# Kernel tuning notes

Measured on AMD Instinct MI355X. Metric: run time of the kernel, lower is better.

## Reference

```python
import jax, jax.numpy as jnp
import numpy as np

N_FEAT = 1024
N_HIDDEN = 31


def _lstm_cell(x, h, c, W_ih, W_hh, b_ih, b_hh):
    # PyTorch LSTMCell: gates ordered i, f, g, o
    gates = x @ W_ih.T + b_ih + h @ W_hh.T + b_hh
    i, f, g, o = jnp.split(gates, 4, axis=-1)
    i = jax.nn.sigmoid(i)
    f = jax.nn.sigmoid(f)
    g = jnp.tanh(g)
    o = jax.nn.sigmoid(o)
    c_new = f * c + i * g
    h_new = o * jnp.tanh(c_new)
    return h_new, c_new


def setup_inputs() -> dict:
    key = jax.random.key(0)
    ks = jax.random.split(key, 12)
    B, T = 64, 512
    s1 = 1.0 / np.sqrt(N_HIDDEN)
    inp = {
        "input": jax.random.normal(ks[0], (B, T, N_FEAT), dtype=jnp.float32),
        "W_ih1": jax.random.uniform(ks[1], (4 * N_HIDDEN, N_FEAT), jnp.float32, -s1, s1),
        "W_hh1": jax.random.uniform(ks[2], (4 * N_HIDDEN, N_HIDDEN), jnp.float32, -s1, s1),
        "b_ih1": jax.random.uniform(ks[3], (4 * N_HIDDEN,), jnp.float32, -s1, s1),
        "b_hh1": jax.random.uniform(ks[4], (4 * N_HIDDEN,), jnp.float32, -s1, s1),
        "W_ih2": jax.random.uniform(ks[5], (4 * N_HIDDEN, N_HIDDEN), jnp.float32, -s1, s1),
        "W_hh2": jax.random.uniform(ks[6], (4 * N_HIDDEN, N_HIDDEN), jnp.float32, -s1, s1),
        "b_ih2": jax.random.uniform(ks[7], (4 * N_HIDDEN,), jnp.float32, -s1, s1),
        "b_hh2": jax.random.uniform(ks[8], (4 * N_HIDDEN,), jnp.float32, -s1, s1),
        "W_lin": jax.random.uniform(ks[9], (N_FEAT, N_HIDDEN), jnp.float32, -s1, s1),
        "b_lin": jax.random.uniform(ks[10], (N_FEAT,), jnp.float32, -s1, s1),
        "future": 16,
    }
    return inp


def reference(input, W_ih1, W_hh1, b_ih1, b_hh1, W_ih2, W_hh2, b_ih2, b_hh2, W_lin, b_lin, future):
    B = input.shape[0]
    h0 = jnp.zeros((B, N_HIDDEN), dtype=input.dtype)
    state0 = (h0, h0, h0, h0)  # h_t, c_t, h_t2, c_t2

    def step(state, x_t):
        h_t, c_t, h_t2, c_t2 = state
        h_t, c_t = _lstm_cell(x_t, h_t, c_t, W_ih1, W_hh1, b_ih1, b_hh1)
        h_t2, c_t2 = _lstm_cell(h_t, h_t2, c_t2, W_ih2, W_hh2, b_ih2, b_hh2)
        out = h_t2 @ W_lin.T + b_lin  # [B, N_FEAT]
        return (h_t, c_t, h_t2, c_t2), out

    # teacher-forced pass over the given sequence
    xs = jnp.swapaxes(input, 0, 1)  # [T, B, F]
    state, outs = jax.lax.scan(step, state0, xs)
    last = outs[-1]

    def fut_step(carry, _):
        state, out = carry
        state, out = step(state, out)
        return (state, out), out

    if future > 0:
        _, fut_outs = jax.lax.scan(fut_step, (state, last), None, length=future)
        outs = jnp.concatenate([outs, fut_outs], axis=0)

    return jnp.swapaxes(outs, 0, 1)  # [B, T+future, N_FEAT]
```

## Files before the change

kernel.cpp:

```cpp
#include <hip/hip_runtime.h>
#include <hip/hip_bf16.h>

#define BB_  64
#define TT_  512
#define FF_  1024
#define HH_  31
#define GG_  124
#define FUT_ 16
#define TTOT_ 528
#define OUT_ROW_ ((size_t)TTOT_ * FF_)

#define PRE1_OFF ((size_t)0)
#define H2A_OFF  (PRE1_OFF + (size_t)TT_*64*128)
#define WT_OFF   (H2A_OFF  + (size_t)TTOT_*64*32)
#define MV_OFF   (WT_OFF   + 31*1024)

__device__ __forceinline__ float rdlane(float v, int k) {
    return __uint_as_float(__builtin_amdgcn_readlane(__float_as_uint(v), k));
}

#define REP31(M) M(0) M(1) M(2) M(3) M(4) M(5) M(6) M(7) M(8) M(9) \
                 M(10) M(11) M(12) M(13) M(14) M(15) M(16) M(17) M(18) M(19) \
                 M(20) M(21) M(22) M(23) M(24) M(25) M(26) M(27) M(28) M(29) M(30)
#define REP16E(M) M(0) M(2) M(4) M(6) M(8) M(10) M(12) M(14) \
                  M(16) M(18) M(20) M(22) M(24) M(26) M(28) M(30)
#define REP15O(M) M(1) M(3) M(5) M(7) M(9) M(11) M(13) M(15) \
                  M(17) M(19) M(21) M(23) M(25) M(27) M(29)

__global__ void k0_prep(const float* __restrict__ Wlin, float* __restrict__ WT) {
    int i = blockIdx.x * 256 + threadIdx.x;
    int j = i / 31;
    int k = i - j * 31;
    WT[k * 1024 + j] = Wlin[i];
}

__global__ __launch_bounds__(64) void k0b_mv(
    const float* __restrict__ Wih1, const float* __restrict__ Wlin,
    const float* __restrict__ blin, float* __restrict__ Mv)
{
    int i = blockIdx.x * 64 + threadIdx.x;
    int g = i >> 5, k = i & 31;
    const float* wr = Wih1 + (size_t)g * FF_;
    float acc = 0.0f;
    if (k < 31) {
#pragma unroll 8
        for (int j = 0; j < FF_; j++) acc += wr[j] * Wlin[j * 31 + k];
    } else {
#pragma unroll 8
        for (int j = 0; j < FF_; j++) acc += wr[j] * blin[j];
    }
    Mv[i] = acc;
}

__global__ __launch_bounds__(256) void k1_pregate(
    const float* __restrict__ X,
    const float* __restrict__ Wih1,
    const float* __restrict__ bih1,
    const float* __restrict__ bhh1,
    float* __restrict__ pre1)
{
    __shared__ __align__(16) float xs[32][64];
    __shared__ __align__(16) float ws[32][128];
    const int tid  = threadIdx.x;
    const int t    = blockIdx.x;
    const int tcol = tid & 31, trow = tid >> 5;
    const int c0 = tcol * 4, r0 = trow * 8;

    float4 acc[8];
#pragma unroll
    for (int r = 0; r < 8; r++) acc[r] = make_float4(0.f, 0.f, 0.f, 0.f);

    for (int kc = 0; kc < 32; ++kc) {
        const int k0 = kc * 32;
#pragma unroll
        for (int p = 0; p < 2; p++) {
            int i = tid + p * 256;
            int r = i >> 3, f = i & 7;
            float4 v = *(const float4*)(X + (size_t)r * TT_ * FF_ + (size_t)t * FF_ + k0 + f * 4);
            xs[f * 4 + 0][r] = v.x; xs[f * 4 + 1][r] = v.y;
            xs[f * 4 + 2][r] = v.z; xs[f * 4 + 3][r] = v.w;
        }
#pragma unroll
        for (int p = 0; p < 4; p++) {
            int i = tid + p * 256;
            int g = i >> 3, f = i & 7;
            float4 v = make_float4(0.f, 0.f, 0.f, 0.f);
            if (g < GG_) v = *(const float4*)(Wih1 + (size_t)g * FF_ + k0 + f * 4);
            ws[f * 4 + 0][g] = v.x; ws[f * 4 + 1][g] = v.y;
            ws[f * 4 + 2][g] = v.z; ws[f * 4 + 3][g] = v.w;
        }
        __syncthreads();
#pragma unroll
        for (int k = 0; k < 32; k++) {
            float4 wv = *(const float4*)&ws[k][c0];
            float4 xa = *(const float4*)&xs[k][r0];
            float4 xb = *(const float4*)&xs[k][r0 + 4];
            float rx[8] = {xa.x, xa.y, xa.z, xa.w, xb.x, xb.y, xb.z, xb.w};
#pragma unroll
            for (int r = 0; r < 8; r++) {
                acc[r].x += rx[r] * wv.x; acc[r].y += rx[r] * wv.y;
                acc[r].z += rx[r] * wv.z; acc[r].w += rx[r] * wv.w;
            }
        }
        __syncthreads();
    }
    float bias[4];
#pragma unroll
    for (int cc = 0; cc < 4; cc++) {
        int c = c0 + cc;
        bias[cc] = (c < GG_) ? (bih1[c] + bhh1[c]) : 0.0f;
    }
#pragma unroll
    for (int r = 0; r < 8; r++) {
        int m = t * 64 + r0 + r;
        float4 o = acc[r];
        o.x += bias[0]; o.y += bias[1]; o.z += bias[2]; o.w += bias[3];
        *(float4*)(pre1 + (size_t)m * 128 + c0) = o;
    }
}

__global__ __attribute__((amdgpu_flat_work_group_size(128, 128), amdgpu_waves_per_eu(1)))
void k2_recur(
    const float* __restrict__ pre1,
    const float* __restrict__ Whh1,
    const float* __restrict__ Wih2,
    const float* __restrict__ Whh2,
    const float* __restrict__ bih1, const float* __restrict__ bhh1,
    const float* __restrict__ bih2, const float* __restrict__ bhh2,
    const float* __restrict__ Mv,
    float* __restrict__ h2a)
{
    __shared__ float gA[2][128];
    __shared__ float g2[2][128];
    const int L  = threadIdx.x;
    const int bb = blockIdx.x;
    const int j  = L & 63;
    const int gc = (L < GG_) ? L : (GG_ - 1);
    const bool isg = (gc >= 62 && gc < 93);
    const bool selhi = (j >= 32);
    const int sidx = selhi ? (j - 32) : j;

#define WLOAD(k) float w1_##k  = Whh1[gc * 31 + k]; \
                 float wi2_##k = Wih2[gc * 31 + k]; \
                 float wh2_##k = Whh2[gc * 31 + k];
    REP31(WLOAD)
#undef WLOAD
#define WPIN(k) asm("" : "+v"(w1_##k), "+v"(wi2_##k), "+v"(wh2_##k));
    REP31(WPIN)
#undef WPIN

    const float b2c = bih2[gc] + bhh2[gc];

    float hv = 0.0f, cv = 0.0f;

    float cur0 = pre1[(size_t)bb * 128 + L];
    float pnxt = pre1[((size_t)1 * 64 + bb) * 128 + L];
    float pnx2 = pre1[((size_t)2 * 64 + bb) * 128 + L];
    {
        float pa0 = cur0, pa1 = 0.0f;
#define DPE(k) { float hk = rdlane(hv, 32 + k); pa0 += w1_##k * hk; }
#define DPO(k) { float hk = rdlane(hv, 32 + k); pa1 += w1_##k * hk; }
        REP16E(DPE)
        REP15O(DPO)
#undef DPE
#undef DPO
        float a = pa0 + pa1;
        float z = isg ? (2.0f * a) : a;
        float s = 1.0f / (1.0f + __expf(-z));
        gA[1][L] = isg ? (2.0f * s - 1.0f) : s;
    }
    __syncthreads();
    {
        const float* gsrc = &gA[1][0];
        float ig = gsrc[sidx];
        float fg = gsrc[sidx + 31];
        float gg = gsrc[sidx + 62];
        float og = gsrc[sidx + 93];
        float cvn = fg * cv + ig * gg;
        float e = __expf(-2.0f * cvn);
        float hvn = og * (2.0f / (1.0f + e) - 1.0f);
        cv = selhi ? cvn : 0.0f;
        hv = selhi ? hvn : 0.0f;
    }

    for (int t = 0; t < TT_ - 1; t++) {
        const int pb = t & 1;
        const float cur = pnxt;
        pnxt = pnx2;
        if (t + 3 < TT_) pnx2 = pre1[((size_t)(t + 3) * 64 + bb) * 128 + L];

        float bi0 = b2c, bi1 = 0.0f, bh0 = 0.0f, bh1 = 0.0f;
        float pa0 = cur, pa1 = 0.0f;
#define DME(k) { float h1k = rdlane(hv, 32 + k); float h2k = rdlane(hv, k); \
                 bi0 += wi2_##k * h1k; bh0 += wh2_##k * h2k; pa0 += w1_##k * h1k; }
#define DMO(k) { float h1k = rdlane(hv, 32 + k); float h2k = rdlane(hv, k); \
                 bi1 += wi2_##k * h1k; bh1 += wh2_##k * h2k; pa1 += w1_##k * h1k; }
        REP16E(DME)
        REP15O(DMO)
#undef DME
#undef DMO
        float b = (bi0 + bi1) + (bh0 + bh1);
        float a = pa0 + pa1;
        {
            float z = isg ? (2.0f * b) : b;
            float s = 1.0f / (1.0f + __expf(-z));
            g2[pb][L] = isg ? (2.0f * s - 1.0f) : s;
        }
        {
            float z = isg ? (2.0f * a) : a;
            float s = 1.0f / (1.0f + __expf(-z));
            gA[pb][L] = isg ? (2.0f * s - 1.0f) : s;
        }
        __syncthreads();
        {
            const float* gsrc = selhi ? &gA[pb][0] : &g2[pb][0];
            float ig = gsrc[sidx];
            float fg = gsrc[sidx + 31];
            float gg = gsrc[sidx + 62];
            float og = gsrc[sidx + 93];
            cv = fg * cv + ig * gg;
            float e = __expf(-2.0f * cv);
            hv = og * (2.0f / (1.0f + e) - 1.0f);
        }
        if (L < HH_) h2a[((size_t)t * 64 + bb) * 32 + L] = hv;
    }

    {
        float bi0 = b2c, bi1 = 0.0f, bh0 = 0.0f, bh1 = 0.0f;
#define DTE(k) { float h1k = rdlane(hv, 32 + k); float h2k = rdlane(hv, k); \
                 bi0 += wi2_##k * h1k; bh0 += wh2_##k * h2k; }
#define DTO(k) { float h1k = rdlane(hv, 32 + k); float h2k = rdlane(hv, k); \
                 bi1 += wi2_##k * h1k; bh1 += wh2_##k * h2k; }
        REP16E(DTE)
        REP15O(DTO)
#undef DTE
#undef DTO
        float b = (bi0 + bi1) + (bh0 + bh1);
        float z = isg ? (2.0f * b) : b;
        float s = 1.0f / (1.0f + __expf(-z));
        g2[1][L] = isg ? (2.0f * s - 1.0f) : s;
    }
    __syncthreads();
    {
        const float* gsrc = &g2[1][0];
        float ig = gsrc[sidx];
        float fg = gsrc[sidx + 31];
        float gg = gsrc[sidx + 62];
        float og = gsrc[sidx + 93];
        float cvn = fg * cv + ig * gg;
        float e = __expf(-2.0f * cvn);
        float hvn = og * (2.0f / (1.0f + e) - 1.0f);
        cv = selhi ? cv : cvn;
        hv = selhi ? hv : hvn;
    }
    if (L < HH_) h2a[((size_t)(TT_ - 1) * 64 + bb) * 32 + L] = hv;

#define MLOAD(k) float m_##k = Mv[gc * 32 + k];
    REP31(MLOAD)
#undef MLOAD
    float m_31 = Mv[gc * 32 + 31];
#define MPIN(k) asm("" : "+v"(m_##k));
    REP31(MPIN)
#undef MPIN
    asm("" : "+v"(m_31));
    const float b1c = bih1[gc] + bhh1[gc];

    for (int sft = 0; sft < FUT_; sft++) {
        float pa0 = b1c + m_31, pa1 = 0.0f;
#define DFE(k) { float h2k = rdlane(hv, k); pa0 += m_##k * h2k; }
#define DFO(k) { float h2k = rdlane(hv, k); pa1 += m_##k * h2k; }
        REP16E(DFE)
        REP15O(DFO)
#undef DFE
#undef DFO
#define DGE(k) { float h1k = rdlane(hv, 32 + k); pa0 += w1_##k * h1k; }
#define DGO(k) { float h1k = rdlane(hv, 32 + k); pa1 += w1_##k * h1k; }
        REP16E(DGE)
        REP15O(DGO)
#undef DGE
#undef DGO
        {
            float a = pa0 + pa1;
            float z = isg ? (2.0f * a) : a;
            float s = 1.0f / (1.0f + __expf(-z));
            gA[0][L] = isg ? (2.0f * s - 1.0f) : s;
        }
        __syncthreads();
        {
            const float* gsrc = &gA[0][0];
            float ig = gsrc[sidx];
            float fg = gsrc[sidx + 31];
            float gg = gsrc[sidx + 62];
            float og = gsrc[sidx + 93];
            float cvn = fg * cv + ig * gg;
            float e = __expf(-2.0f * cvn);
            float hvn = og * (2.0f / (1.0f + e) - 1.0f);
            cv = selhi ? cvn : cv;
            hv = selhi ? hvn : hv;
        }
        float bi0 = b2c, bi1 = 0.0f, bh0 = 0.0f, bh1 = 0.0f;
#define DHE(k) { float h1k = rdlane(hv, 32 + k); float h2k = rdlane(hv, k); \
                 bi0 += wi2_##k * h1k; bh0 += wh2_##k * h2k; }
#define DHO(k) { float h1k = rdlane(hv, 32 + k); float h2k = rdlane(hv, k); \
                 bi1 += wi2_##k * h1k; bh1 += wh2_##k * h2k; }
        REP16E(DHE)
        REP15O(DHO)
#undef DHE
#undef DHO
        {
            float b = (bi0 + bi1) + (bh0 + bh1);
            float z = isg ? (2.0f * b) : b;
            float s = 1.0f / (1.0f + __expf(-z));
            g2[0][L] = isg ? (2.0f * s - 1.0f) : s;
        }
        __syncthreads();
        {
            const float* gsrc = &g2[0][0];
            float ig = gsrc[sidx];
            float fg = gsrc[sidx + 31];
            float gg = gsrc[sidx + 62];
            float og = gsrc[sidx + 93];
            float cvn = fg * cv + ig * gg;
            float e = __expf(-2.0f * cvn);
            float hvn = og * (2.0f / (1.0f + e) - 1.0f);
            cv = selhi ? cv : cvn;
            hv = selhi ? hv : hvn;
        }
        if (L < HH_) h2a[((size_t)(TT_ + sft) * 64 + bb) * 32 + L] = hv;
    }
}

__global__ __launch_bounds__(256) void k3_outlin(
    const float* __restrict__ h2a,
    const float* __restrict__ WT,
    const float* __restrict__ blin,
    float* __restrict__ out)
{
    __shared__ __align__(16) float hl[16][32];
    const int tid = threadIdx.x;
    const int m0  = blockIdx.x * 16;
#pragma unroll
    for (int p = 0; p < 2; p++) {
        int i = tid + p * 256;
        int r = i >> 5, k = i & 31;
        hl[r][k] = h2a[(size_t)(m0 + r) * 32 + k];
    }
    __syncthreads();
    const int c0 = tid * 4;
    float4 bl = *(const float4*)(blin + c0);
    float4 acc[16];
#pragma unroll
    for (int r = 0; r < 16; r++) acc[r] = bl;
    for (int k = 0; k < 31; k++) {
        float4 wv = *(const float4*)(WT + k * 1024 + c0);
#pragma unroll
        for (int r = 0; r < 16; r++) {
            float h = hl[r][k];
            acc[r].x += h * wv.x; acc[r].y += h * wv.y;
            acc[r].z += h * wv.z; acc[r].w += h * wv.w;
        }
    }
    const int t  = m0 >> 6;
    const int b0 = m0 & 63;
#pragma unroll
    for (int r = 0; r < 16; r++) {
        int b = b0 + r;
        *(float4*)(out + (size_t)b * OUT_ROW_ + (size_t)t * FF_ + c0) = acc[r];
    }
}

extern "C" void kernel_launch(void* const* d_in, const int* in_sizes, int n_in,
                              void* d_out, int out_size, void* d_ws, size_t ws_size,
                              hipStream_t stream) {
    (void)in_sizes; (void)n_in; (void)out_size; (void)ws_size;
    const float* X    = (const float*)d_in[0];
    const float* Wih1 = (const float*)d_in[1];
    const float* Whh1 = (const float*)d_in[2];
    const float* bih1 = (const float*)d_in[3];
    const float* bhh1 = (const float*)d_in[4];
    const float* Wih2 = (const float*)d_in[5];
    const float* Whh2 = (const float*)d_in[6];
    const float* bih2 = (const float*)d_in[7];
    const float* bhh2 = (const float*)d_in[8];
    const float* Wlin = (const float*)d_in[9];
    const float* blin = (const float*)d_in[10];

    float* ws   = (float*)d_ws;
    float* pre1 = ws + PRE1_OFF;
    float* h2a  = ws + H2A_OFF;
    float* WT   = ws + WT_OFF;
    float* Mv   = ws + MV_OFF;
    float* out  = (float*)d_out;

    hipLaunchKernelGGL(k0_prep,    dim3(124),  dim3(256), 0, stream, Wlin, WT);
    hipLaunchKernelGGL(k0b_mv,     dim3(62),   dim3(64),  0, stream, Wih1, Wlin, blin, Mv);
    hipLaunchKernelGGL(k1_pregate, dim3(TT_),  dim3(256), 0, stream, X, Wih1, bih1, bhh1, pre1);
    hipLaunchKernelGGL(k2_recur,   dim3(BB_),  dim3(128), 0, stream, pre1, Whh1, Wih2, Whh2,
                       bih1, bhh1, bih2, bhh2, Mv, h2a);
    hipLaunchKernelGGL(k3_outlin,  dim3(TTOT_*4), dim3(256), 0, stream, h2a, WT, blin, out);
}
```

Measured before the change: 809.9 us.

## Pack four batch rows per workgroup in the LSTM recurrence kernel

The recurrent kernel now runs 16 workgroups of 512 threads, each handling four independent batch rows with per-row shared gate buffers, instead of 64 workgroups of 128 threads. The intent is to put more waves on each CU so that latency in the serial readlane/FMA/exp chain can be overlapped across batch rows. The cost is that work is concentrated on fewer CUs, so several waves share each SIMD's issue slots. Every block-wide barrier now waits on all eight waves. The new launch bounds may also cap VGPRs below the roughly 125 pinned weight registers per thread, which risks spills.

```diff
diff --git a/kernel.cpp b/kernel.cpp
--- a/kernel.cpp
+++ b/kernel.cpp
@@ -119,8 +119,7 @@
     }
 }
 
-__global__ __attribute__((amdgpu_flat_work_group_size(128, 128), amdgpu_waves_per_eu(1)))
-void k2_recur(
+__global__ __launch_bounds__(512, 2) void k2_recur(
     const float* __restrict__ pre1,
     const float* __restrict__ Whh1,
     const float* __restrict__ Wih2,
@@ -130,12 +129,14 @@
     const float* __restrict__ Mv,
     float* __restrict__ h2a)
 {
-    __shared__ float gA[2][128];
-    __shared__ float g2[2][128];
-    const int L  = threadIdx.x;
-    const int bb = blockIdx.x;
-    const int j  = L & 63;
-    const int gc = (L < GG_) ? L : (GG_ - 1);
+    __shared__ float gA[4][2][128];
+    __shared__ float g2[4][2][128];
+    const int Lall = threadIdx.x;
+    const int bsl  = Lall >> 7;
+    const int L    = Lall & 127;
+    const int bb   = blockIdx.x * 4 + bsl;
+    const int j    = L & 63;
+    const int gc   = (L < GG_) ? L : (GG_ - 1);
     const bool isg = (gc >= 62 && gc < 93);
     const bool selhi = (j >= 32);
     const int sidx = selhi ? (j - 32) : j;
@@ -167,11 +168,11 @@
         float a = pa0 + pa1;
         float z = isg ? (2.0f * a) : a;
         float s = 1.0f / (1.0f + __expf(-z));
-        gA[1][L] = isg ? (2.0f * s - 1.0f) : s;
+        gA[bsl][1][L] = isg ? (2.0f * s - 1.0f) : s;
     }
     __syncthreads();
     {
-        const float* gsrc = &gA[1][0];
+        const float* gsrc = &gA[bsl][1][0];
         float ig = gsrc[sidx];
         float fg = gsrc[sidx + 31];
         float gg = gsrc[sidx + 62];
@@ -204,16 +205,16 @@
         {
             float z = isg ? (2.0f * b) : b;
             float s = 1.0f / (1.0f + __expf(-z));
-            g2[pb][L] = isg ? (2.0f * s - 1.0f) : s;
+            g2[bsl][pb][L] = isg ? (2.0f * s - 1.0f) : s;
         }
         {
             float z = isg ? (2.0f * a) : a;
             float s = 1.0f / (1.0f + __expf(-z));
-            gA[pb][L] = isg ? (2.0f * s - 1.0f) : s;
+            gA[bsl][pb][L] = isg ? (2.0f * s - 1.0f) : s;
         }
         __syncthreads();
         {
-            const float* gsrc = selhi ? &gA[pb][0] : &g2[pb][0];
+            const float* gsrc = selhi ? &gA[bsl][pb][0] : &g2[bsl][pb][0];
             float ig = gsrc[sidx];
             float fg = gsrc[sidx + 31];
             float gg = gsrc[sidx + 62];
@@ -238,11 +239,11 @@
         float b = (bi0 + bi1) + (bh0 + bh1);
         float z = isg ? (2.0f * b) : b;
         float s = 1.0f / (1.0f + __expf(-z));
-        g2[1][L] = isg ? (2.0f * s - 1.0f) : s;
+        g2[bsl][1][L] = isg ? (2.0f * s - 1.0f) : s;
     }
     __syncthreads();
     {
-        const float* gsrc = &g2[1][0];
+        const float* gsrc = &g2[bsl][1][0];
         float ig = gsrc[sidx];
         float fg = gsrc[sidx + 31];
         float gg = gsrc[sidx + 62];
@@ -283,11 +284,11 @@
             float a = pa0 + pa1;
             float z = isg ? (2.0f * a) : a;
             float s = 1.0f / (1.0f + __expf(-z));
-            gA[0][L] = isg ? (2.0f * s - 1.0f) : s;
+            gA[bsl][0][L] = isg ? (2.0f * s - 1.0f) : s;
         }
         __syncthreads();
         {
-            const float* gsrc = &gA[0][0];
+            const float* gsrc = &gA[bsl][0][0];
             float ig = gsrc[sidx];
             float fg = gsrc[sidx + 31];
             float gg = gsrc[sidx + 62];
@@ -311,11 +312,11 @@
             float b = (bi0 + bi1) + (bh0 + bh1);
             float z = isg ? (2.0f * b) : b;
             float s = 1.0f / (1.0f + __expf(-z));
-            g2[0][L] = isg ? (2.0f * s - 1.0f) : s;
+            g2[bsl][0][L] = isg ? (2.0f * s - 1.0f) : s;
         }
         __syncthreads();
         {
-            const float* gsrc = &g2[0][0];
+            const float* gsrc = &g2[bsl][0][0];
             float ig = gsrc[sidx];
             float fg = gsrc[sidx + 31];
             float gg = gsrc[sidx + 62];
@@ -395,7 +396,7 @@
     hipLaunchKernelGGL(k0_prep,    dim3(124),  dim3(256), 0, stream, Wlin, WT);
     hipLaunchKernelGGL(k0b_mv,     dim3(62),   dim3(64),  0, stream, Wih1, Wlin, blin, Mv);
     hipLaunchKernelGGL(k1_pregate, dim3(TT_),  dim3(256), 0, stream, X, Wih1, bih1, bhh1, pre1);
-    hipLaunchKernelGGL(k2_recur,   dim3(BB_),  dim3(128), 0, stream, pre1, Whh1, Wih2, Whh2,
+    hipLaunchKernelGGL(k2_recur,   dim3(BB_/4), dim3(512), 0, stream, pre1, Whh1, Wih2, Whh2,
                        bih1, bhh1, bih2, bhh2, Mv, h2a);
     hipLaunchKernelGGL(k3_outlin,  dim3(TTOT_*4), dim3(256), 0, stream, h2a, WT, blin, out);
 }
```

Measured after the change: 939.7 us. 1.16x slower.

## Fuse prep kernels into pregate launch and enlarge GEMM and output-linear tiles

Applied to the files above, without the earlier changes.

Merges the Wlin transpose, the Mv precompute and the input pregate GEMM into one heterogeneous launch, using block ranges to dispatch the different roles. The pregate GEMM now handles two timesteps per block with 8 output columns per thread, so each loaded Wih1 tile is reused across twice as many rows. The output linear kernel processes 32 rows per block instead of 16. The aim is fewer launches and more weight reuse, at the cost of higher register pressure (64 and 128 accumulator floats) and fewer blocks for parallelism.

```diff
diff --git a/kernel.cpp b/kernel.cpp
--- a/kernel.cpp
+++ b/kernel.cpp
@@ -27,95 +27,107 @@
 #define REP15O(M) M(1) M(3) M(5) M(7) M(9) M(11) M(13) M(15) \
                   M(17) M(19) M(21) M(23) M(25) M(27) M(29)
 
-__global__ void k0_prep(const float* __restrict__ Wlin, float* __restrict__ WT) {
-    int i = blockIdx.x * 256 + threadIdx.x;
-    int j = i / 31;
-    int k = i - j * 31;
-    WT[k * 1024 + j] = Wlin[i];
-}
-
-__global__ __launch_bounds__(64) void k0b_mv(
-    const float* __restrict__ Wih1, const float* __restrict__ Wlin,
-    const float* __restrict__ blin, float* __restrict__ Mv)
-{
-    int i = blockIdx.x * 64 + threadIdx.x;
-    int g = i >> 5, k = i & 31;
-    const float* wr = Wih1 + (size_t)g * FF_;
-    float acc = 0.0f;
-    if (k < 31) {
-#pragma unroll 8
-        for (int j = 0; j < FF_; j++) acc += wr[j] * Wlin[j * 31 + k];
-    } else {
-#pragma unroll 8
-        for (int j = 0; j < FF_; j++) acc += wr[j] * blin[j];
-    }
-    Mv[i] = acc;
-}
-
-__global__ __launch_bounds__(256) void k1_pregate(
+__global__ __launch_bounds__(256) void k_front(
     const float* __restrict__ X,
     const float* __restrict__ Wih1,
     const float* __restrict__ bih1,
     const float* __restrict__ bhh1,
-    float* __restrict__ pre1)
+    const float* __restrict__ Wlin,
+    const float* __restrict__ blin,
+    float* __restrict__ pre1,
+    float* __restrict__ WT,
+    float* __restrict__ Mv)
 {
-    __shared__ __align__(16) float xs[32][64];
+    __shared__ __align__(16) float xs[32][128];
     __shared__ __align__(16) float ws[32][128];
-    const int tid  = threadIdx.x;
-    const int t    = blockIdx.x;
-    const int tcol = tid & 31, trow = tid >> 5;
-    const int c0 = tcol * 4, r0 = trow * 8;
-
-    float4 acc[8];
-#pragma unroll
-    for (int r = 0; r < 8; r++) acc[r] = make_float4(0.f, 0.f, 0.f, 0.f);
-
-    for (int kc = 0; kc < 32; ++kc) {
-        const int k0 = kc * 32;
-#pragma unroll
-        for (int p = 0; p < 2; p++) {
-            int i = tid + p * 256;
-            int r = i >> 3, f = i & 7;
-            float4 v = *(const float4*)(X + (size_t)r * TT_ * FF_ + (size_t)t * FF_ + k0 + f * 4);
-            xs[f * 4 + 0][r] = v.x; xs[f * 4 + 1][r] = v.y;
-            xs[f * 4 + 2][r] = v.z; xs[f * 4 + 3][r] = v.w;
-        }
-#pragma unroll
-        for (int p = 0; p < 4; p++) {
-            int i = tid + p * 256;
-            int g = i >> 3, f = i & 7;
-            float4 v = make_float4(0.f, 0.f, 0.f, 0.f);
-            if (g < GG_) v = *(const float4*)(Wih1 + (size_t)g * FF_ + k0 + f * 4);
-            ws[f * 4 + 0][g] = v.x; ws[f * 4 + 1][g] = v.y;
-            ws[f * 4 + 2][g] = v.z; ws[f * 4 + 3][g] = v.w;
-        }
-        __syncthreads();
-#pragma unroll
-        for (int k = 0; k < 32; k++) {
-            float4 wv = *(const float4*)&ws[k][c0];
-            float4 xa = *(const float4*)&xs[k][r0];
-            float4 xb = *(const float4*)&xs[k][r0 + 4];
-            float rx[8] = {xa.x, xa.y, xa.z, xa.w, xb.x, xb.y, xb.z, xb.w};
-#pragma unroll
-            for (int r = 0; r < 8; r++) {
-                acc[r].x += rx[r] * wv.x; acc[r].y += rx[r] * wv.y;
-                acc[r].z += rx[r] * wv.z; acc[r].w += rx[r] * wv.w;
+    const int blk = blockIdx.x;
+    const int tid = threadIdx.x;
+
+    if (blk < 256) {
+        const int t0   = blk * 2;
+        const int tcol = tid & 15, trow = tid >> 4;
+        const int c0 = tcol * 8, r0 = trow * 8;
+
+        float4 a0[8], a1[8];
+#pragma unroll
+        for (int r = 0; r < 8; r++) { a0[r] = make_float4(0.f,0.f,0.f,0.f); a1[r] = a0[r]; }
+
+        for (int kc = 0; kc < 32; ++kc) {
+            const int k0f = kc * 32;
+#pragma unroll
+            for (int p = 0; p < 4; p++) {
+                int i = tid + p * 256;
+                int r = i >> 3, f = i & 7;
+                int bb = r & 63, tt = t0 + (r >> 6);
+                float4 v = *(const float4*)(X + (size_t)bb * TT_ * FF_ + (size_t)tt * FF_ + k0f + f * 4);
+                xs[f * 4 + 0][r] = v.x; xs[f * 4 + 1][r] = v.y;
+                xs[f * 4 + 2][r] = v.z; xs[f * 4 + 3][r] = v.w;
             }
-        }
-        __syncthreads();
-    }
-    float bias[4];
-#pragma unroll
-    for (int cc = 0; cc < 4; cc++) {
-        int c = c0 + cc;
-        bias[cc] = (c < GG_) ? (bih1[c] + bhh1[c]) : 0.0f;
-    }
-#pragma unroll
-    for (int r = 0; r < 8; r++) {
-        int m = t * 64 + r0 + r;
-        float4 o = acc[r];
-        o.x += bias[0]; o.y += bias[1]; o.z += bias[2]; o.w += bias[3];
-        *(float4*)(pre1 + (size_t)m * 128 + c0) = o;
+#pragma unroll
+            for (int p = 0; p < 4; p++) {
+                int i = tid + p * 256;
+                int g = i >> 3, f = i & 7;
+                float4 v = make_float4(0.f, 0.f, 0.f, 0.f);
+                if (g < GG_) v = *(const float4*)(Wih1 + (size_t)g * FF_ + k0f + f * 4);
+                ws[f * 4 + 0][g] = v.x; ws[f * 4 + 1][g] = v.y;
+                ws[f * 4 + 2][g] = v.z; ws[f * 4 + 3][g] = v.w;
+            }
+            __syncthreads();
+#pragma unroll
+            for (int k = 0; k < 32; k++) {
+                float4 wv0 = *(const float4*)&ws[k][c0];
+                float4 wv1 = *(const float4*)&ws[k][c0 + 4];
+                float4 xa  = *(const float4*)&xs[k][r0];
+                float4 xb  = *(const float4*)&xs[k][r0 + 4];
+                float rx[8] = {xa.x, xa.y, xa.z, xa.w, xb.x, xb.y, xb.z, xb.w};
+#pragma unroll
+                for (int r = 0; r < 8; r++) {
+                    a0[r].x += rx[r] * wv0.x; a0[r].y += rx[r] * wv0.y;
+                    a0[r].z += rx[r] * wv0.z; a0[r].w += rx[r] * wv0.w;
+                    a1[r].x += rx[r] * wv1.x; a1[r].y += rx[r] * wv1.y;
+                    a1[r].z += rx[r] * wv1.z; a1[r].w += rx[r] * wv1.w;
+                }
+            }
+            __syncthreads();
+        }
+        float bias0[4], bias1[4];
+#pragma unroll
+        for (int cc = 0; cc < 4; cc++) {
+            int c = c0 + cc;
+            bias0[cc] = (c < GG_) ? (bih1[c] + bhh1[c]) : 0.0f;
+            c = c0 + 4 + cc;
+            bias1[cc] = (c < GG_) ? (bih1[c] + bhh1[c]) : 0.0f;
+        }
+#pragma unroll
+        for (int r = 0; r < 8; r++) {
+            int row = r0 + r;
+            int m = (t0 + (row >> 6)) * 64 + (row & 63);
+            float4 o0 = a0[r], o1 = a1[r];
+            o0.x += bias0[0]; o0.y += bias0[1]; o0.z += bias0[2]; o0.w += bias0[3];
+            o1.x += bias1[0]; o1.y += bias1[1]; o1.z += bias1[2]; o1.w += bias1[3];
+            *(float4*)(pre1 + (size_t)m * 128 + c0)     = o0;
+            *(float4*)(pre1 + (size_t)m * 128 + c0 + 4) = o1;
+        }
+    } else if (blk < 380) {
+        int i = (blk - 256) * 256 + tid;
+        int j = i / 31;
+        int k = i - j * 31;
+        WT[k * 1024 + j] = Wlin[i];
+    } else {
+        int idx = (blk - 380) * 256 + tid;
+        if (idx < GG_ * 32) {
+            int g = idx >> 5, k = idx & 31;
+            const float* wr = Wih1 + (size_t)g * FF_;
+            float acc = 0.0f;
+            if (k < 31) {
+#pragma unroll 8
+                for (int j = 0; j < FF_; j++) acc += wr[j] * Wlin[j * 31 + k];
+            } else {
+#pragma unroll 8
+                for (int j = 0; j < FF_; j++) acc += wr[j] * blin[j];
+            }
+            Mv[idx] = acc;
+        }
     }
 }
 
@@ -336,11 +348,11 @@
     const float* __restrict__ blin,
     float* __restrict__ out)
 {
-    __shared__ __align__(16) float hl[16][32];
+    __shared__ __align__(16) float hl[32][32];
     const int tid = threadIdx.x;
-    const int m0  = blockIdx.x * 16;
-#pragma unroll
-    for (int p = 0; p < 2; p++) {
+    const int m0  = blockIdx.x * 32;
+#pragma unroll
+    for (int p = 0; p < 4; p++) {
         int i = tid + p * 256;
         int r = i >> 5, k = i & 31;
         hl[r][k] = h2a[(size_t)(m0 + r) * 32 + k];
@@ -348,13 +360,13 @@
     __syncthreads();
     const int c0 = tid * 4;
     float4 bl = *(const float4*)(blin + c0);
-    float4 acc[16];
-#pragma unroll
-    for (int r = 0; r < 16; r++) acc[r] = bl;
+    float4 acc[32];
+#pragma unroll
+    for (int r = 0; r < 32; r++) acc[r] = bl;
     for (int k = 0; k < 31; k++) {
         float4 wv = *(const float4*)(WT + k * 1024 + c0);
 #pragma unroll
-        for (int r = 0; r < 16; r++) {
+        for (int r = 0; r < 32; r++) {
             float h = hl[r][k];
             acc[r].x += h * wv.x; acc[r].y += h * wv.y;
             acc[r].z += h * wv.z; acc[r].w += h * wv.w;
@@ -363,7 +375,7 @@
     const int t  = m0 >> 6;
     const int b0 = m0 & 63;
 #pragma unroll
-    for (int r = 0; r < 16; r++) {
+    for (int r = 0; r < 32; r++) {
         int b = b0 + r;
         *(float4*)(out + (size_t)b * OUT_ROW_ + (size_t)t * FF_ + c0) = acc[r];
     }
@@ -392,10 +404,9 @@
     float* Mv   = ws + MV_OFF;
     float* out  = (float*)d_out;
 
-    hipLaunchKernelGGL(k0_prep,    dim3(124),  dim3(256), 0, stream, Wlin, WT);
-    hipLaunchKernelGGL(k0b_mv,     dim3(62),   dim3(64),  0, stream, Wih1, Wlin, blin, Mv);
-    hipLaunchKernelGGL(k1_pregate, dim3(TT_),  dim3(256), 0, stream, X, Wih1, bih1, bhh1, pre1);
-    hipLaunchKernelGGL(k2_recur,   dim3(BB_),  dim3(128), 0, stream, pre1, Whh1, Wih2, Whh2,
+    hipLaunchKernelGGL(k_front,   dim3(396),    dim3(256), 0, stream,
+                       X, Wih1, bih1, bhh1, Wlin, blin, pre1, WT, Mv);
+    hipLaunchKernelGGL(k2_recur,  dim3(BB_),    dim3(128), 0, stream, pre1, Whh1, Wih2, Whh2,
                        bih1, bhh1, bih2, bhh2, Mv, h2a);
-    hipLaunchKernelGGL(k3_outlin,  dim3(TTOT_*4), dim3(256), 0, stream, h2a, WT, blin, out);
+    hipLaunchKernelGGL(k3_outlin, dim3(TTOT_*2), dim3(256), 0, stream, h2a, WT, blin, out);
 }
```

Result: faster. 776.8 us (-4.1%).

## Fuse pregate GEMM and recurrence into one kernel with flag-based overlap

Applied to the files above, without the earlier changes.

Merges the weight-prep, Mv precompute, input pregate GEMM and LSTM recurrence into one launch. Blocks 0-511 produce pregates per timestep and signal per-group atomic counters with release semantics. Blocks 512-575 run the recurrence and spin on those counters, so the sequential recurrence can start while later pregates are still being computed. This removes the serialization between the GEMM and the recurrence and cuts launch count. The output-projection kernel is also retiled to 32 rows per block. The risks are spin-wait overhead, consumer-before-producer scheduling hazards, and register pressure from the 256-thread launch bound on the recurrence path.

```diff
diff --git a/kernel.cpp b/kernel.cpp
--- a/kernel.cpp
+++ b/kernel.cpp
@@ -14,9 +14,20 @@
 #define H2A_OFF  (PRE1_OFF + (size_t)TT_*64*128)
 #define WT_OFF   (H2A_OFF  + (size_t)TTOT_*64*32)
 #define MV_OFF   (WT_OFF   + 31*1024)
+#define FLG_OFF  (MV_OFF   + 124*32)
+
+#define NPROD 512
+#define KBLK  64
+#define NBLK  (NPROD + KBLK)
 
 __device__ __forceinline__ float rdlane(float v, int k) {
     return __uint_as_float(__builtin_amdgcn_readlane(__float_as_uint(v), k));
+}
+__device__ __forceinline__ int aload_acq(int* p) {
+    return __hip_atomic_load(p, __ATOMIC_ACQUIRE, __HIP_MEMORY_SCOPE_AGENT);
+}
+__device__ __forceinline__ void aadd_rel(int* p, int v) {
+    __hip_atomic_fetch_add(p, v, __ATOMIC_RELEASE, __HIP_MEMORY_SCOPE_AGENT);
 }
 
 #define REP31(M) M(0) M(1) M(2) M(3) M(4) M(5) M(6) M(7) M(8) M(9) \
@@ -27,267 +38,174 @@
 #define REP15O(M) M(1) M(3) M(5) M(7) M(9) M(11) M(13) M(15) \
                   M(17) M(19) M(21) M(23) M(25) M(27) M(29)
 
-__global__ void k0_prep(const float* __restrict__ Wlin, float* __restrict__ WT) {
-    int i = blockIdx.x * 256 + threadIdx.x;
-    int j = i / 31;
-    int k = i - j * 31;
-    WT[k * 1024 + j] = Wlin[i];
-}
-
-__global__ __launch_bounds__(64) void k0b_mv(
-    const float* __restrict__ Wih1, const float* __restrict__ Wlin,
-    const float* __restrict__ blin, float* __restrict__ Mv)
-{
-    int i = blockIdx.x * 64 + threadIdx.x;
-    int g = i >> 5, k = i & 31;
-    const float* wr = Wih1 + (size_t)g * FF_;
-    float acc = 0.0f;
-    if (k < 31) {
-#pragma unroll 8
-        for (int j = 0; j < FF_; j++) acc += wr[j] * Wlin[j * 31 + k];
-    } else {
-#pragma unroll 8
-        for (int j = 0; j < FF_; j++) acc += wr[j] * blin[j];
-    }
-    Mv[i] = acc;
-}
-
-__global__ __launch_bounds__(256) void k1_pregate(
+__global__ void k_zero(int* flg) {
+    if (threadIdx.x < 128) flg[threadIdx.x] = 0;
+}
+
+__global__ __launch_bounds__(256) void k_fused(
     const float* __restrict__ X,
     const float* __restrict__ Wih1,
-    const float* __restrict__ bih1,
-    const float* __restrict__ bhh1,
-    float* __restrict__ pre1)
-{
-    __shared__ __align__(16) float xs[32][64];
-    __shared__ __align__(16) float ws[32][128];
-    const int tid  = threadIdx.x;
-    const int t    = blockIdx.x;
-    const int tcol = tid & 31, trow = tid >> 5;
-    const int c0 = tcol * 4, r0 = trow * 8;
-
-    float4 acc[8];
-#pragma unroll
-    for (int r = 0; r < 8; r++) acc[r] = make_float4(0.f, 0.f, 0.f, 0.f);
-
-    for (int kc = 0; kc < 32; ++kc) {
-        const int k0 = kc * 32;
-#pragma unroll
-        for (int p = 0; p < 2; p++) {
-            int i = tid + p * 256;
-            int r = i >> 3, f = i & 7;
-            float4 v = *(const float4*)(X + (size_t)r * TT_ * FF_ + (size_t)t * FF_ + k0 + f * 4);
-            xs[f * 4 + 0][r] = v.x; xs[f * 4 + 1][r] = v.y;
-            xs[f * 4 + 2][r] = v.z; xs[f * 4 + 3][r] = v.w;
-        }
-#pragma unroll
-        for (int p = 0; p < 4; p++) {
-            int i = tid + p * 256;
-            int g = i >> 3, f = i & 7;
-            float4 v = make_float4(0.f, 0.f, 0.f, 0.f);
-            if (g < GG_) v = *(const float4*)(Wih1 + (size_t)g * FF_ + k0 + f * 4);
-            ws[f * 4 + 0][g] = v.x; ws[f * 4 + 1][g] = v.y;
-            ws[f * 4 + 2][g] = v.z; ws[f * 4 + 3][g] = v.w;
-        }
-        __syncthreads();
-#pragma unroll
-        for (int k = 0; k < 32; k++) {
-            float4 wv = *(const float4*)&ws[k][c0];
-            float4 xa = *(const float4*)&xs[k][r0];
-            float4 xb = *(const float4*)&xs[k][r0 + 4];
-            float rx[8] = {xa.x, xa.y, xa.z, xa.w, xb.x, xb.y, xb.z, xb.w};
-#pragma unroll
-            for (int r = 0; r < 8; r++) {
-                acc[r].x += rx[r] * wv.x; acc[r].y += rx[r] * wv.y;
-                acc[r].z += rx[r] * wv.z; acc[r].w += rx[r] * wv.w;
-            }
-        }
-        __syncthreads();
-    }
-    float bias[4];
-#pragma unroll
-    for (int cc = 0; cc < 4; cc++) {
-        int c = c0 + cc;
-        bias[cc] = (c < GG_) ? (bih1[c] + bhh1[c]) : 0.0f;
-    }
-#pragma unroll
-    for (int r = 0; r < 8; r++) {
-        int m = t * 64 + r0 + r;
-        float4 o = acc[r];
-        o.x += bias[0]; o.y += bias[1]; o.z += bias[2]; o.w += bias[3];
-        *(float4*)(pre1 + (size_t)m * 128 + c0) = o;
-    }
-}
-
-__global__ __attribute__((amdgpu_flat_work_group_size(128, 128), amdgpu_waves_per_eu(1)))
-void k2_recur(
-    const float* __restrict__ pre1,
     const float* __restrict__ Whh1,
     const float* __restrict__ Wih2,
     const float* __restrict__ Whh2,
     const float* __restrict__ bih1, const float* __restrict__ bhh1,
     const float* __restrict__ bih2, const float* __restrict__ bhh2,
-    const float* __restrict__ Mv,
-    float* __restrict__ h2a)
+    const float* __restrict__ Wlin,
+    const float* __restrict__ blin,
+    float* __restrict__ pre1,
+    float* __restrict__ h2a,
+    float* __restrict__ WT,
+    float* __restrict__ Mv,
+    int*   __restrict__ flg)
 {
-    __shared__ float gA[2][128];
-    __shared__ float g2[2][128];
-    const int L  = threadIdx.x;
-    const int bb = blockIdx.x;
-    const int j  = L & 63;
-    const int gc = (L < GG_) ? L : (GG_ - 1);
-    const bool isg = (gc >= 62 && gc < 93);
-    const bool selhi = (j >= 32);
-    const int sidx = selhi ? (j - 32) : j;
+    __shared__ __align__(16) float smem[6144];
+    int* pre_grp = flg;
+    int* mv_cnt  = flg + 64;
+    const int blk = blockIdx.x;
+    const int tid = threadIdx.x;
+
+    if (blk < NPROD) {
+        const int t = blk;
+        {
+            float (*xs)[64]  = (float(*)[64])smem;
+            float (*ws)[128] = (float(*)[128])(smem + 2048);
+            const int tcol = tid & 31, trow = tid >> 5;
+            const int c0 = tcol * 4, r0 = trow * 8;
+
+            float4 acc[8];
+#pragma unroll
+            for (int r = 0; r < 8; r++) acc[r] = make_float4(0.f, 0.f, 0.f, 0.f);
+
+            for (int kc = 0; kc < 32; ++kc) {
+                const int k0 = kc * 32;
+#pragma unroll
+                for (int p = 0; p < 2; p++) {
+                    int i = tid + p * 256;
+                    int r = i >> 3, f = i & 7;
+                    float4 v = *(const float4*)(X + (size_t)r * TT_ * FF_ + (size_t)t * FF_ + k0 + f * 4);
+                    xs[f * 4 + 0][r] = v.x; xs[f * 4 + 1][r] = v.y;
+                    xs[f * 4 + 2][r] = v.z; xs[f * 4 + 3][r] = v.w;
+                }
+#pragma unroll
+                for (int p = 0; p < 4; p++) {
+                    int i = tid + p * 256;
+                    int g = i >> 3, f = i & 7;
+                    float4 v = make_float4(0.f, 0.f, 0.f, 0.f);
+                    if (g < GG_) v = *(const float4*)(Wih1 + (size_t)g * FF_ + k0 + f * 4);
+                    ws[f * 4 + 0][g] = v.x; ws[f * 4 + 1][g] = v.y;
+                    ws[f * 4 + 2][g] = v.z; ws[f * 4 + 3][g] = v.w;
+                }
+                __syncthreads();
+#pragma unroll
+                for (int k = 0; k < 32; k++) {
+                    float4 wv = *(const float4*)&ws[k][c0];
+                    float4 xa = *(const float4*)&xs[k][r0];
+                    float4 xb = *(const float4*)&xs[k][r0 + 4];
+                    float rx[8] = {xa.x, xa.y, xa.z, xa.w, xb.x, xb.y, xb.z, xb.w};
+#pragma unroll
+                    for (int r = 0; r < 8; r++) {
+                        acc[r].x += rx[r] * wv.x; acc[r].y += rx[r] * wv.y;
+                        acc[r].z += rx[r] * wv.z; acc[r].w += rx[r] * wv.w;
+                    }
+                }
+                __syncthreads();
+            }
+            float bias[4];
+#pragma unroll
+            for (int cc = 0; cc < 4; cc++) {
+                int c = c0 + cc;
+                bias[cc] = (c < GG_) ? (bih1[c] + bhh1[c]) : 0.0f;
+            }
+#pragma unroll
+            for (int r = 0; r < 8; r++) {
+                int m = t * 64 + r0 + r;
+                float4 o = acc[r];
+                o.x += bias[0]; o.y += bias[1]; o.z += bias[2]; o.w += bias[3];
+                *(float4*)(pre1 + (size_t)m * 128 + c0) = o;
+            }
+        }
+        __syncthreads();
+        if (tid == 0) aadd_rel(&pre_grp[t >> 3], 1);
+
+        if (t < 124) {
+            int i = t * 256 + tid;
+            int j = i / 31;
+            int k = i - j * 31;
+            WT[k * 1024 + j] = Wlin[i];
+        } else if (t < 140) {
+            int idx = (t - 124) * 256 + tid;
+            if (idx < GG_ * 32) {
+                int g = idx >> 5, k = idx & 31;
+                const float* wr = Wih1 + (size_t)g * FF_;
+                float acc = 0.0f;
+                if (k < 31) {
+#pragma unroll 8
+                    for (int j = 0; j < FF_; j++) acc += wr[j] * Wlin[j * 31 + k];
+                } else {
+#pragma unroll 8
+                    for (int j = 0; j < FF_; j++) acc += wr[j] * blin[j];
+                }
+                Mv[idx] = acc;
+            }
+            __syncthreads();
+            if (tid == 0) aadd_rel(mv_cnt, 1);
+        }
+        return;
+    }
+
+    if (tid >= 128) {
+        __syncthreads();
+        for (int t = 0; t < TT_ - 1; t++) __syncthreads();
+        __syncthreads();
+        for (int s = 0; s < FUT_; s++) { __syncthreads(); __syncthreads(); }
+        return;
+    }
+
+    {
+        const int L  = tid;
+        const int bb = blk - NPROD;
+        const int j  = L & 63;
+        const int gc = (L < GG_) ? L : (GG_ - 1);
+        const bool isg = (gc >= 62 && gc < 93);
+        const bool selhi = (j >= 32);
+        const int sidx = selhi ? (j - 32) : j;
+        float (*gA)[128] = (float(*)[128])smem;
+        float (*g2)[128] = (float(*)[128])(smem + 256);
 
 #define WLOAD(k) float w1_##k  = Whh1[gc * 31 + k]; \
                  float wi2_##k = Wih2[gc * 31 + k]; \
                  float wh2_##k = Whh2[gc * 31 + k];
-    REP31(WLOAD)
+        REP31(WLOAD)
 #undef WLOAD
 #define WPIN(k) asm("" : "+v"(w1_##k), "+v"(wi2_##k), "+v"(wh2_##k));
-    REP31(WPIN)
+        REP31(WPIN)
 #undef WPIN
 
-    const float b2c = bih2[gc] + bhh2[gc];
-
-    float hv = 0.0f, cv = 0.0f;
-
-    float cur0 = pre1[(size_t)bb * 128 + L];
-    float pnxt = pre1[((size_t)1 * 64 + bb) * 128 + L];
-    float pnx2 = pre1[((size_t)2 * 64 + bb) * 128 + L];
-    {
-        float pa0 = cur0, pa1 = 0.0f;
+        const float b2c = bih2[gc] + bhh2[gc];
+        float hv = 0.0f, cv = 0.0f;
+        int rg = 0;
+
+        while (aload_acq(&pre_grp[0]) < 8) __builtin_amdgcn_s_sleep(8);
+        rg = 1;
+        float cur0 = pre1[(size_t)bb * 128 + L];
+        float pnxt = pre1[((size_t)1 * 64 + bb) * 128 + L];
+        float pnx2 = pre1[((size_t)2 * 64 + bb) * 128 + L];
+        {
+            float pa0 = cur0, pa1 = 0.0f;
 #define DPE(k) { float hk = rdlane(hv, 32 + k); pa0 += w1_##k * hk; }
 #define DPO(k) { float hk = rdlane(hv, 32 + k); pa1 += w1_##k * hk; }
-        REP16E(DPE)
-        REP15O(DPO)
+            REP16E(DPE)
+            REP15O(DPO)
 #undef DPE
 #undef DPO
-        float a = pa0 + pa1;
-        float z = isg ? (2.0f * a) : a;
-        float s = 1.0f / (1.0f + __expf(-z));
-        gA[1][L] = isg ? (2.0f * s - 1.0f) : s;
-    }
-    __syncthreads();
-    {
-        const float* gsrc = &gA[1][0];
-        float ig = gsrc[sidx];
-        float fg = gsrc[sidx + 31];
-        float gg = gsrc[sidx + 62];
-        float og = gsrc[sidx + 93];
-        float cvn = fg * cv + ig * gg;
-        float e = __expf(-2.0f * cvn);
-        float hvn = og * (2.0f / (1.0f + e) - 1.0f);
-        cv = selhi ? cvn : 0.0f;
-        hv = selhi ? hvn : 0.0f;
-    }
-
-    for (int t = 0; t < TT_ - 1; t++) {
-        const int pb = t & 1;
-        const float cur = pnxt;
-        pnxt = pnx2;
-        if (t + 3 < TT_) pnx2 = pre1[((size_t)(t + 3) * 64 + bb) * 128 + L];
-
-        float bi0 = b2c, bi1 = 0.0f, bh0 = 0.0f, bh1 = 0.0f;
-        float pa0 = cur, pa1 = 0.0f;
-#define DME(k) { float h1k = rdlane(hv, 32 + k); float h2k = rdlane(hv, k); \
-                 bi0 += wi2_##k * h1k; bh0 += wh2_##k * h2k; pa0 += w1_##k * h1k; }
-#define DMO(k) { float h1k = rdlane(hv, 32 + k); float h2k = rdlane(hv, k); \
-                 bi1 += wi2_##k * h1k; bh1 += wh2_##k * h2k; pa1 += w1_##k * h1k; }
-        REP16E(DME)
-        REP15O(DMO)
-#undef DME
-#undef DMO
-        float b = (bi0 + bi1) + (bh0 + bh1);
-        float a = pa0 + pa1;
-        {
-            float z = isg ? (2.0f * b) : b;
-            float s = 1.0f / (1.0f + __expf(-z));
-            g2[pb][L] = isg ? (2.0f * s - 1.0f) : s;
-        }
-        {
-            float z = isg ? (2.0f * a) : a;
-            float s = 1.0f / (1.0f + __expf(-z));
-            gA[pb][L] = isg ? (2.0f * s - 1.0f) : s;
-        }
-        __syncthreads();
-        {
-            const float* gsrc = selhi ? &gA[pb][0] : &g2[pb][0];
-            float ig = gsrc[sidx];
-            float fg = gsrc[sidx + 31];
-            float gg = gsrc[sidx + 62];
-            float og = gsrc[sidx + 93];
-            cv = fg * cv + ig * gg;
-            float e = __expf(-2.0f * cv);
-            hv = og * (2.0f / (1.0f + e) - 1.0f);
-        }
-        if (L < HH_) h2a[((size_t)t * 64 + bb) * 32 + L] = hv;
-    }
-
-    {
-        float bi0 = b2c, bi1 = 0.0f, bh0 = 0.0f, bh1 = 0.0f;
-#define DTE(k) { float h1k = rdlane(hv, 32 + k); float h2k = rdlane(hv, k); \
-                 bi0 += wi2_##k * h1k; bh0 += wh2_##k * h2k; }
-#define DTO(k) { float h1k = rdlane(hv, 32 + k); float h2k = rdlane(hv, k); \
-                 bi1 += wi2_##k * h1k; bh1 += wh2_##k * h2k; }
-        REP16E(DTE)
-        REP15O(DTO)
-#undef DTE
-#undef DTO
-        float b = (bi0 + bi1) + (bh0 + bh1);
-        float z = isg ? (2.0f * b) : b;
-        float s = 1.0f / (1.0f + __expf(-z));
-        g2[1][L] = isg ? (2.0f * s - 1.0f) : s;
-    }
-    __syncthreads();
-    {
-        const float* gsrc = &g2[1][0];
-        float ig = gsrc[sidx];
-        float fg = gsrc[sidx + 31];
-        float gg = gsrc[sidx + 62];
-        float og = gsrc[sidx + 93];
-        float cvn = fg * cv + ig * gg;
-        float e = __expf(-2.0f * cvn);
-        float hvn = og * (2.0f / (1.0f + e) - 1.0f);
-        cv = selhi ? cv : cvn;
-        hv = selhi ? hv : hvn;
-    }
-    if (L < HH_) h2a[((size_t)(TT_ - 1) * 64 + bb) * 32 + L] = hv;
-
-#define MLOAD(k) float m_##k = Mv[gc * 32 + k];
-    REP31(MLOAD)
-#undef MLOAD
-    float m_31 = Mv[gc * 32 + 31];
-#define MPIN(k) asm("" : "+v"(m_##k));
-    REP31(MPIN)
-#undef MPIN
-    asm("" : "+v"(m_31));
-    const float b1c = bih1[gc] + bhh1[gc];
-
-    for (int sft = 0; sft < FUT_; sft++) {
-        float pa0 = b1c + m_31, pa1 = 0.0f;
-#define DFE(k) { float h2k = rdlane(hv, k); pa0 += m_##k * h2k; }
-#define DFO(k) { float h2k = rdlane(hv, k); pa1 += m_##k * h2k; }
-        REP16E(DFE)
-        REP15O(DFO)
-#undef DFE
-#undef DFO
-#define DGE(k) { float h1k = rdlane(hv, 32 + k); pa0 += w1_##k * h1k; }
-#define DGO(k) { float h1k = rdlane(hv, 32 + k); pa1 += w1_##k * h1k; }
-        REP16E(DGE)
-        REP15O(DGO)
-#undef DGE
-#undef DGO
-        {
             float a = pa0 + pa1;
             float z = isg ? (2.0f * a) : a;
             float s = 1.0f / (1.0f + __expf(-z));
-            gA[0][L] = isg ? (2.0f * s - 1.0f) : s;
+            gA[1][L] = isg ? (2.0f * s - 1.0f) : s;
         }
         __syncthreads();
         {
-            const float* gsrc = &gA[0][0];
+            const float* gsrc = &gA[1][0];
             float ig = gsrc[sidx];
             float fg = gsrc[sidx + 31];
             float gg = gsrc[sidx + 62];
@@ -295,27 +213,77 @@
             float cvn = fg * cv + ig * gg;
             float e = __expf(-2.0f * cvn);
             float hvn = og * (2.0f / (1.0f + e) - 1.0f);
-            cv = selhi ? cvn : cv;
-            hv = selhi ? hvn : hv;
-        }
-        float bi0 = b2c, bi1 = 0.0f, bh0 = 0.0f, bh1 = 0.0f;
-#define DHE(k) { float h1k = rdlane(hv, 32 + k); float h2k = rdlane(hv, k); \
+            cv = selhi ? cvn : 0.0f;
+            hv = selhi ? hvn : 0.0f;
+        }
+
+        for (int t = 0; t < TT_ - 1; t++) {
+            const int pb = t & 1;
+            const float cur = pnxt;
+            pnxt = pnx2;
+            if (t + 3 < TT_) {
+                const int gneed = (t + 3) >> 3;
+                while (rg <= gneed) {
+                    if (aload_acq(&pre_grp[rg]) == 8) rg++;
+                    else __builtin_amdgcn_s_sleep(2);
+                }
+                pnx2 = pre1[((size_t)(t + 3) * 64 + bb) * 128 + L];
+            }
+
+            float bi0 = b2c, bi1 = 0.0f, bh0 = 0.0f, bh1 = 0.0f;
+            float pa0 = cur, pa1 = 0.0f;
+#define DME(k) { float h1k = rdlane(hv, 32 + k); float h2k = rdlane(hv, k); \
+                 bi0 += wi2_##k * h1k; bh0 += wh2_##k * h2k; pa0 += w1_##k * h1k; }
+#define DMO(k) { float h1k = rdlane(hv, 32 + k); float h2k = rdlane(hv, k); \
+                 bi1 += wi2_##k * h1k; bh1 += wh2_##k * h2k; pa1 += w1_##k * h1k; }
+            REP16E(DME)
+            REP15O(DMO)
+#undef DME
+#undef DMO
+            float b = (bi0 + bi1) + (bh0 + bh1);
+            float a = pa0 + pa1;
+            {
+                float z = isg ? (2.0f * b) : b;
+                float s = 1.0f / (1.0f + __expf(-z));
+                g2[pb][L] = isg ? (2.0f * s - 1.0f) : s;
+            }
+            {
+                float z = isg ? (2.0f * a) : a;
+                float s = 1.0f / (1.0f + __expf(-z));
+                gA[pb][L] = isg ? (2.0f * s - 1.0f) : s;
+            }
+            __syncthreads();
+            {
+                const float* gsrc = selhi ? &gA[pb][0] : &g2[pb][0];
+                float ig = gsrc[sidx];
+                float fg = gsrc[sidx + 31];
+                float gg = gsrc[sidx + 62];
+                float og = gsrc[sidx + 93];
+                cv = fg * cv + ig * gg;
+                float e = __expf(-2.0f * cv);
+                hv = og * (2.0f / (1.0f + e) - 1.0f);
+            }
+            if (L < HH_) h2a[((size_t)t * 64 + bb) * 32 + L] = hv;
+        }
+
+        {
+            float bi0 = b2c, bi1 = 0.0f, bh0 = 0.0f, bh1 = 0.0f;
+#define DTE(k) { float h1k = rdlane(hv, 32 + k); float h2k = rdlane(hv, k); \
                  bi0 += wi2_##k * h1k; bh0 += wh2_##k * h2k; }
-#define DHO(k) { float h1k = rdlane(hv, 32 + k); float h2k = rdlane(hv, k); \
+#define DTO(k) { float h1k = rdlane(hv, 32 + k); float h2k = rdlane(hv, k); \
                  bi1 += wi2_##k * h1k; bh1 += wh2_##k * h2k; }
-        REP16E(DHE)
-        REP15O(DHO)
-#undef DHE
-#undef DHO
-        {
+            REP16E(DTE)
+            REP15O(DTO)
+#undef DTE
+#undef DTO
             float b = (bi0 + bi1) + (bh0 + bh1);
             float z = isg ? (2.0f * b) : b;
             float s = 1.0f / (1.0f + __expf(-z));
-            g2[0][L] = isg ? (2.0f * s - 1.0f) : s;
+            g2[1][L] = isg ? (2.0f * s - 1.0f) : s;
         }
         __syncthreads();
         {
-            const float* gsrc = &g2[0][0];
+            const float* gsrc = &g2[1][0];
             float ig = gsrc[sidx];
             float fg = gsrc[sidx + 31];
             float gg = gsrc[sidx + 62];
@@ -326,7 +294,82 @@
             cv = selhi ? cv : cvn;
             hv = selhi ? hv : hvn;
         }
-        if (L < HH_) h2a[((size_t)(TT_ + sft) * 64 + bb) * 32 + L] = hv;
+        if (L < HH_) h2a[((size_t)(TT_ - 1) * 64 + bb) * 32 + L] = hv;
+
+        while (aload_acq(mv_cnt) < 16) __builtin_amdgcn_s_sleep(2);
+#define MLOAD(k) float m_##k = Mv[gc * 32 + k];
+        REP31(MLOAD)
+#undef MLOAD
+        float m_31 = Mv[gc * 32 + 31];
+#define MPIN(k) asm("" : "+v"(m_##k));
+        REP31(MPIN)
+#undef MPIN
+        asm("" : "+v"(m_31));
+        const float b1c = bih1[gc] + bhh1[gc];
+
+        for (int sft = 0; sft < FUT_; sft++) {
+            float pa0 = b1c + m_31, pa1 = 0.0f;
+#define DFE(k) { float h2k = rdlane(hv, k); pa0 += m_##k * h2k; }
+#define DFO(k) { float h2k = rdlane(hv, k); pa1 += m_##k * h2k; }
+            REP16E(DFE)
+            REP15O(DFO)
+#undef DFE
+#undef DFO
+#define DGE(k) { float h1k = rdlane(hv, 32 + k); pa0 += w1_##k * h1k; }
+#define DGO(k) { float h1k = rdlane(hv, 32 + k); pa1 += w1_##k * h1k; }
+            REP16E(DGE)
+            REP15O(DGO)
+#undef DGE
+#undef DGO
+            {
+                float a = pa0 + pa1;
+                float z = isg ? (2.0f * a) : a;
+                float s = 1.0f / (1.0f + __expf(-z));
+                gA[0][L] = isg ? (2.0f * s - 1.0f) : s;
+            }
+            __syncthreads();
+            {
+                const float* gsrc = &gA[0][0];
+                float ig = gsrc[sidx];
+                float fg = gsrc[sidx + 31];
+                float gg = gsrc[sidx + 62];
+                float og = gsrc[sidx + 93];
+                float cvn = fg * cv + ig * gg;
+                float e = __expf(-2.0f * cvn);
+                float hvn = og * (2.0f / (1.0f + e) - 1.0f);
+                cv = selhi ? cvn : cv;
+                hv = selhi ? hvn : hv;
+            }
+            float bi0 = b2c, bi1 = 0.0f, bh0 = 0.0f, bh1 = 0.0f;
+#define DHE(k) { float h1k = rdlane(hv, 32 + k); float h2k = rdlane(hv, k); \
+                 bi0 += wi2_##k * h1k; bh0 += wh2_##k * h2k; }
+#define DHO(k) { float h1k = rdlane(hv, 32 + k); float h2k = rdlane(hv, k); \
+                 bi1 += wi2_##k * h1k; bh1 += wh2_##k * h2k; }
+            REP16E(DHE)
+            REP15O(DHO)
+#undef DHE
+#undef DHO
+            {
+                float b = (bi0 + bi1) + (bh0 + bh1);
+                float z = isg ? (2.0f * b) : b;
+                float s = 1.0f / (1.0f + __expf(-z));
+                g2[0][L] = isg ? (2.0f * s - 1.0f) : s;
+            }
+            __syncthreads();
+            {
+                const float* gsrc = &g2[0][0];
+                float ig = gsrc[sidx];
+                float fg = gsrc[sidx + 31];
+                float gg = gsrc[sidx + 62];
+                float og = gsrc[sidx + 93];
+                float cvn = fg * cv + ig * gg;
+                float e = __expf(-2.0f * cvn);
+                float hvn = og * (2.0f / (1.0f + e) - 1.0f);
+                cv = selhi ? cv : cvn;
+                hv = selhi ? hv : hvn;
+            }
+            if (L < HH_) h2a[((size_t)(TT_ + sft) * 64 + bb) * 32 + L] = hv;
+        }
     }
 }
 
@@ -336,11 +379,11 @@
     const float* __restrict__ blin,
     float* __restrict__ out)
 {
-    __shared__ __align__(16) float hl[16][32];
+    __shared__ __align__(16) float hl[32][32];
     const int tid = threadIdx.x;
-    const int m0  = blockIdx.x * 16;
-#pragma unroll
-    for (int p = 0; p < 2; p++) {
+    const int m0  = blockIdx.x * 32;
+#pragma unroll
+    for (int p = 0; p < 4; p++) {
         int i = tid + p * 256;
         int r = i >> 5, k = i & 31;
         hl[r][k] = h2a[(size_t)(m0 + r) * 32 + k];
@@ -348,13 +391,13 @@
     __syncthreads();
     const int c0 = tid * 4;
     float4 bl = *(const float4*)(blin + c0);
-    float4 acc[16];
-#pragma unroll
-    for (int r = 0; r < 16; r++) acc[r] = bl;
+    float4 acc[32];
+#pragma unroll
+    for (int r = 0; r < 32; r++) acc[r] = bl;
     for (int k = 0; k < 31; k++) {
         float4 wv = *(const float4*)(WT + k * 1024 + c0);
 #pragma unroll
-        for (int r = 0; r < 16; r++) {
+        for (int r = 0; r < 32; r++) {
             float h = hl[r][k];
             acc[r].x += h * wv.x; acc[r].y += h * wv.y;
             acc[r].z += h * wv.z; acc[r].w += h * wv.w;
@@ -363,7 +406,7 @@
     const int t  = m0 >> 6;
     const int b0 = m0 & 63;
 #pragma unroll
-    for (int r = 0; r < 16; r++) {
+    for (int r = 0; r < 32; r++) {
         int b = b0 + r;
         *(float4*)(out + (size_t)b * OUT_ROW_ + (size_t)t * FF_ + c0) = acc[r];
     }
@@ -390,12 +433,12 @@
     float* h2a  = ws + H2A_OFF;
     float* WT   = ws + WT_OFF;
     float* Mv   = ws + MV_OFF;
+    int*   flg  = (int*)(ws + FLG_OFF);
     float* out  = (float*)d_out;
 
-    hipLaunchKernelGGL(k0_prep,    dim3(124),  dim3(256), 0, stream, Wlin, WT);
-    hipLaunchKernelGGL(k0b_mv,     dim3(62),   dim3(64),  0, stream, Wih1, Wlin, blin, Mv);
-    hipLaunchKernelGGL(k1_pregate, dim3(TT_),  dim3(256), 0, stream, X, Wih1, bih1, bhh1, pre1);
-    hipLaunchKernelGGL(k2_recur,   dim3(BB_),  dim3(128), 0, stream, pre1, Whh1, Wih2, Whh2,
-                       bih1, bhh1, bih2, bhh2, Mv, h2a);
-    hipLaunchKernelGGL(k3_outlin,  dim3(TTOT_*4), dim3(256), 0, stream, h2a, WT, blin, out);
-}
+    hipLaunchKernelGGL(k_zero,  dim3(1),       dim3(256), 0, stream, flg);
+    hipLaunchKernelGGL(k_fused, dim3(NBLK),    dim3(256), 0, stream,
+                       X, Wih1, Whh1, Wih2, Whh2, bih1, bhh1, bih2, bhh2,
+                       Wlin, blin, pre1, h2a, WT, Mv, flg);
+    hipLaunchKernelGGL(k3_outlin, dim3(TTOT_*2), dim3(256), 0, stream, h2a, WT, blin, out);
+}
```

New measurement: 864.5 us. +6.7%, slower.
